# Kernel optimization log

Hardware: AMD Instinct MI355X
Metric: run time of the kernel (lower is better)

The kernel has to match this reference:

```python
import jax, jax.numpy as jnp
import numpy as np

EPS = 1e-5
C = 6          # channels (attention length)
H = 2          # heads

def _ln(x, w, b):
    mu = jnp.mean(x, axis=-1, keepdims=True)
    var = jnp.var(x, axis=-1, keepdims=True)
    return (x - mu) * jax.lax.rsqrt(var + EPS) * w + b

def setup_inputs() -> dict:
    B, N, D = 8, 4096, 768
    S = D // C           # slot_dim = 128
    key = jax.random.key(0)
    ks = jax.random.split(key, 16)
    std = 1.0 / np.sqrt(S)
    return {
        "x": jax.random.normal(ks[0], (B, N, D), jnp.float32),
        "norm1_w": jnp.ones((D,), jnp.float32),
        "norm1_b": jnp.zeros((D,), jnp.float32),
        "norm2_w": jnp.ones((S,), jnp.float32),
        "norm2_b": jnp.zeros((S,), jnp.float32),
        "qw": jax.random.normal(ks[1], (S, S), jnp.float32) * std,
        "qb": jnp.zeros((S,), jnp.float32),
        "kw": jax.random.normal(ks[2], (S, S), jnp.float32) * std,
        "kb": jnp.zeros((S,), jnp.float32),
        "vw": jax.random.normal(ks[3], (S, S), jnp.float32) * std,
        "vb": jnp.zeros((S,), jnp.float32),
        "ow": jax.random.normal(ks[4], (S, S), jnp.float32) * std,
        "ob": jnp.zeros((S,), jnp.float32),
        "ff1w": jax.random.normal(ks[5], (S, 4 * S), jnp.float32) * std,
        "ff1b": jnp.zeros((4 * S,), jnp.float32),
        "ff2w": jax.random.normal(ks[6], (4 * S, S), jnp.float32) * (std / 2),
        "ff2b": jnp.zeros((S,), jnp.float32),
    }

def reference(x, norm1_w, norm1_b, norm2_w, norm2_b,
              qw, qb, kw, kb, vw, vb, ow, ob,
              ff1w, ff1b, ff2w, ff2b):
    B, N, D = x.shape
    S = D // C
    hd = S // H
    scale = hd ** -0.5

    residual = x
    xn = _ln(x, norm1_w, norm1_b)                       # (B,N,D)
    xf = xn.reshape(B * N, C, S)                        # (M,C,S)
    xf = _ln(xf, norm2_w, norm2_b)

    # MHA over C=6 channel tokens per (B*N) slot
    M = B * N
    q = (xf @ qw + qb).reshape(M, C, H, hd)
    k = (xf @ kw + kb).reshape(M, C, H, hd)
    v = (xf @ vw + vb).reshape(M, C, H, hd)
    attn = jnp.einsum('mqhd,mkhd->mhqk', q, k) * scale  # (M,H,C,C)
    attn = jax.nn.softmax(attn, axis=-1)
    o = jnp.einsum('mhqk,mkhd->mqhd', attn, v).reshape(M, C, S)
    att_out = o @ ow + ob

    xf = xf + att_out
    ff_in = xf
    h = _ln(xf, norm2_w, norm2_b)                       # same norm2 params reused
    h = jax.nn.gelu(h @ ff1w + ff1b, approximate=False) @ ff2w + ff2b
    xf = ff_in + h

    return residual + xf.reshape(B, N, D)
```

## Files before the change

### kernel.cpp

```cpp
#include <hip/hip_runtime.h>
#include <hip/hip_bf16.h>

typedef unsigned short u16;
typedef unsigned int u32;
using bf16x8 = __attribute__((ext_vector_type(8))) short;
using f32x4  = __attribute__((ext_vector_type(4))) float;

#define LDA   136
#define SLOTS 16
#define NROWS 96

__device__ __forceinline__ u32 pk2bf(float a, float b) {
  u32 r;
  asm("v_cvt_pk_bf16_f32 %0, %1, %2" : "=v"(r) : "v"(a), "v"(b));
  return r;
}
__device__ __forceinline__ u16 f2bf(float f) { return (u16)pk2bf(f, f); }
__device__ __forceinline__ float bf2f(u16 h) {
  union { u32 u; float f; } v; v.u = ((u32)h) << 16;
  return v.f;
}
__device__ __forceinline__ float2 bf2x2(u32 u) {
  union { u32 u; float f; } a, b; a.u = u << 16; b.u = u & 0xffff0000u;
  return make_float2(a.f, b.f);
}

#if __has_builtin(__builtin_amdgcn_exp2f)
#define EXP2F(x) __builtin_amdgcn_exp2f(x)
#else
#define EXP2F(x) exp2f(x)
#endif

#define MFMA32(a, b, c) __builtin_amdgcn_mfma_f32_16x16x32_bf16(a, b, c, 0, 0, 0)

__device__ __forceinline__ float gelu_f(float x) {
  const float a = x * x;
  const float b = fmaf(-0.10294538f, a, -2.3022077f);
  const float e = EXP2F(x * b);
  return x * __builtin_amdgcn_rcpf(1.f + e);
}

__device__ __forceinline__ void handoff() {
  __builtin_amdgcn_sched_barrier(0x7F);
  asm volatile("s_waitcnt lgkmcnt(0)" ::: "memory");
  __builtin_amdgcn_sched_barrier(0x7F);
}

__global__ void convert_w(const float* __restrict__ qw, const float* __restrict__ kw,
                          const float* __restrict__ vw, const float* __restrict__ ow,
                          const float* __restrict__ f1, const float* __restrict__ f2,
                          u16* __restrict__ o) {
  int i = blockIdx.x * 256 + threadIdx.x;
  if (i < 65536) {
    int which = i >> 14;
    const float* W = which == 0 ? qw : which == 1 ? kw : which == 2 ? vw : ow;
    int t = i & 16383;
    int n = t >> 7, k = t & 127;
    o[i] = f2bf(W[k * 128 + n]);
  } else if (i < 131072) {
    int t = i - 65536;
    int n = t >> 7, k = t & 127;
    o[i] = f2bf(f1[k * 512 + n]);
  } else if (i < 196608) {
    int t = i - 131072;
    int n = t >> 9, k = t & 511;
    o[i] = f2bf(f2[k * 128 + n]);
  }
}

__device__ __forceinline__ void gemm96(const u16* __restrict__ A, const u16* __restrict__ WT,
                                       int ldw, f32x4 acc[6],
                                       int wave, int lane16, int kgrp) {
#pragma unroll
  for (int ks = 0; ks < 4; ++ks) {
    const int kk = ks * 32 + kgrp * 8;
    const bf16x8 b = *(const bf16x8*)(WT + (wave * 16 + lane16) * ldw + kk);
    __builtin_amdgcn_s_setprio(1);
#pragma unroll
    for (int xr = 0; xr < 6; ++xr) {
      const bf16x8 a = *(const bf16x8*)(A + (xr * 16 + lane16) * LDA + kk);
      acc[xr] = MFMA32(b, a, acc[xr]);
    }
    __builtin_amdgcn_s_setprio(0);
  }
}

__device__ __forceinline__ void store96(u16* __restrict__ dst, f32x4 acc[6],
                                        const float* __restrict__ bias,
                                        int wave, int lane16, int kgrp) {
  const int col0 = wave * 16 + kgrp * 4;
  const float4 bv = *(const float4*)(bias + col0);
#pragma unroll
  for (int xr = 0; xr < 6; ++xr) {
    uint2 o;
    o.x = pk2bf(acc[xr][0] + bv.x, acc[xr][1] + bv.y);
    o.y = pk2bf(acc[xr][2] + bv.z, acc[xr][3] + bv.w);
    *(uint2*)(dst + (xr * 16 + lane16) * LDA + col0) = o;
  }
}

__global__ __launch_bounds__(512) void mitra_main(
    const float* __restrict__ x,
    const float* __restrict__ nw1, const float* __restrict__ nb1,
    const float* __restrict__ nw2, const float* __restrict__ nb2,
    const float* __restrict__ qb,  const float* __restrict__ kb,
    const float* __restrict__ vb,  const float* __restrict__ ob,
    const float* __restrict__ f1b, const float* __restrict__ f2b,
    const u16* __restrict__ wt, float* __restrict__ out) {
  __shared__ u16 XF[NROWS * LDA];
  __shared__ u16 BA[NROWS * LDA];
  __shared__ u16 BB[NROWS * LDA];
  __shared__ u16 PS2[2 * NROWS * 8];

  const int tid    = threadIdx.x;
  const int wave   = tid >> 6;
  const int lane   = tid & 63;
  const int lane16 = lane & 15;
  const int kgrp   = lane >> 4;
  const long slot0 = (long)blockIdx.x * SLOTS;

#pragma unroll
  for (int si = 0; si < 2; ++si) {
    const int s = wave + si * 8;
    const float* xr = x + (size_t)(slot0 + s) * 768;
    const int l32 = lane & 31;
    float4 v[3];
    float sm = 0.f, sq = 0.f;
#pragma unroll
    for (int p = 0; p < 3; ++p) {
      v[p] = *(const float4*)(xr + (p * 64 + lane) * 4);
      sm += v[p].x + v[p].y + v[p].z + v[p].w;
      sq += v[p].x * v[p].x + v[p].y * v[p].y + v[p].z * v[p].z + v[p].w * v[p].w;
    }
#pragma unroll
    for (int m = 1; m < 64; m <<= 1) { sm += __shfl_xor(sm, m); sq += __shfl_xor(sq, m); }
    const float mu = sm * (1.f / 768.f);
    const float rs = rsqrtf(sq * (1.f / 768.f) - mu * mu + 1e-5f);
#pragma unroll
    for (int p = 0; p < 3; ++p) {
      const float4 w = *(const float4*)(nw1 + (p * 64 + lane) * 4);
      const float4 b = *(const float4*)(nb1 + (p * 64 + lane) * 4);
      v[p].x = (v[p].x - mu) * rs * w.x + b.x;
      v[p].y = (v[p].y - mu) * rs * w.y + b.y;
      v[p].z = (v[p].z - mu) * rs * w.z + b.z;
      v[p].w = (v[p].w - mu) * rs * w.w + b.w;
    }
    const float4 w2 = *(const float4*)(nw2 + l32 * 4);
    const float4 b2 = *(const float4*)(nb2 + l32 * 4);
#pragma unroll
    for (int p = 0; p < 3; ++p) {
      float s2 = v[p].x + v[p].y + v[p].z + v[p].w;
      float q2 = v[p].x * v[p].x + v[p].y * v[p].y + v[p].z * v[p].z + v[p].w * v[p].w;
#pragma unroll
      for (int m = 1; m < 32; m <<= 1) { s2 += __shfl_xor(s2, m); q2 += __shfl_xor(q2, m); }
      const float mu2 = s2 * (1.f / 128.f);
      const float rs2 = rsqrtf(q2 * (1.f / 128.f) - mu2 * mu2 + 1e-5f);
      const int row = s * 6 + 2 * p + (lane >> 5);
      uint2 o;
      o.x = pk2bf((v[p].x - mu2) * rs2 * w2.x + b2.x, (v[p].y - mu2) * rs2 * w2.y + b2.y);
      o.y = pk2bf((v[p].z - mu2) * rs2 * w2.z + b2.z, (v[p].w - mu2) * rs2 * w2.w + b2.w);
      *(uint2*)(XF + row * LDA + l32 * 4) = o;
    }
  }
  __syncthreads();

  {
    f32x4 acc[6] = {};
    gemm96(XF, wt + 0, 128, acc, wave, lane16, kgrp);
    store96(BA, acc, qb, wave, lane16, kgrp);
  }
  {
    f32x4 acc[6] = {};
    gemm96(XF, wt + 16384, 128, acc, wave, lane16, kgrp);
    store96(BB, acc, kb, wave, lane16, kgrp);
  }
  __syncthreads();

  {
#pragma unroll
    for (int jl = 0; jl < 4; ++jl) {
      const int j = wave + jl * 8;
      if (j < 28) {
        const int h  = j & 1;
        const int tt = j >> 1;
        int qt, kt;
        if (tt < 6) { qt = tt; kt = tt; }
        else {
          const int idx  = tt - 6;
          const int base = idx >> 1;
          const int lo   = base + (base >> 1);
          const int dir  = idx & 1;
          qt = lo + dir; kt = lo + 1 - dir;
        }
        f32x4 acc = {};
#pragma unroll
        for (int ks = 0; ks < 2; ++ks) {
          const int kk = h * 64 + ks * 32 + kgrp * 8;
          const bf16x8 kf = *(const bf16x8*)(BB + (kt * 16 + lane16) * LDA + kk);
          const bf16x8 qf = *(const bf16x8*)(BA + (qt * 16 + lane16) * LDA + kk);
          acc = MFMA32(kf, qf, acc);
        }
        const int q    = qt * 16 + lane16;
        const int klo  = 6 * ((unsigned)q / 6u);
        u16* pq = PS2 + (h * NROWS + q) * 8;
#pragma unroll
        for (int r = 0; r < 4; ++r) {
          const int off = kt * 16 + kgrp * 4 + r - klo;
          if ((unsigned)off < 6u) pq[off] = f2bf(acc[r] * 0.125f);
        }
      }
    }
  }
  __syncthreads();

  {
    f32x4 acc[6] = {};
    gemm96(XF, wt + 32768, 128, acc, wave, lane16, kgrp);
    store96(BA, acc, vb, wave, lane16, kgrp);
  }
  __syncthreads();

  {
    if (lane < 24) {
      const int h  = lane / 12;
      const int q  = wave * 12 + (lane % 12);
      u16* pr = PS2 + (h * NROWS + q) * 8;
      float e[6];
      float m = bf2f(pr[0]);
#pragma unroll
      for (int k = 1; k < 6; ++k) m = fmaxf(m, bf2f(pr[k]));
      float ssum = 0.f;
#pragma unroll
      for (int k = 0; k < 6; ++k) { e[k] = EXP2F((bf2f(pr[k]) - m) * 1.44269504f); ssum += e[k]; }
      const float inv = __builtin_amdgcn_rcpf(ssum);
#pragma unroll
      for (int k = 0; k < 6; ++k) pr[k] = f2bf(e[k] * inv);
    }
    handoff();

    const int dseg = lane & 15;
    const int d0   = dseg * 8;
    const int h    = dseg >> 3;
    const int rgrp = lane >> 4;
#pragma unroll
    for (int p = 0; p < 3; ++p) {
      const int rl = rgrp * 3 + p;
      const int q  = wave * 12 + rl;
      const int sl = rl / 6;
      const u16* pr = PS2 + (h * NROWS + q) * 8;
      const u16* vbase = BA + (wave * 12 + sl * 6) * LDA + d0;
      float o0 = 0, o1 = 0, o2 = 0, o3 = 0, o4 = 0, o5 = 0, o6 = 0, o7 = 0;
#pragma unroll
      for (int k = 0; k < 6; ++k) {
        const uint4 v4 = *(const uint4*)(vbase + k * LDA);
        const float pw = bf2f(pr[k]);
        const float2 a = bf2x2(v4.x), b = bf2x2(v4.y);
        const float2 c = bf2x2(v4.z), d = bf2x2(v4.w);
        o0 = fmaf(pw, a.x, o0); o1 = fmaf(pw, a.y, o1);
        o2 = fmaf(pw, b.x, o2); o3 = fmaf(pw, b.y, o3);
        o4 = fmaf(pw, c.x, o4); o5 = fmaf(pw, c.y, o5);
        o6 = fmaf(pw, d.x, o6); o7 = fmaf(pw, d.y, o7);
      }
      uint4 o;
      o.x = pk2bf(o0, o1); o.y = pk2bf(o2, o3);
      o.z = pk2bf(o4, o5); o.w = pk2bf(o6, o7);
      *(uint4*)(BB + q * LDA + d0) = o;
    }
  }
  __syncthreads();

  {
    f32x4 acc[6] = {};
    gemm96(BB, wt + 49152, 128, acc, wave, lane16, kgrp);
    const int col0 = wave * 16 + kgrp * 4;
    const float4 bv = *(const float4*)(ob + col0);
#pragma unroll
    for (int xr = 0; xr < 6; ++xr) {
      u16* px = XF + (xr * 16 + lane16) * LDA + col0;
      const uint2 cur = *(const uint2*)px;
      const float2 lo = bf2x2(cur.x), hi = bf2x2(cur.y);
      uint2 o;
      o.x = pk2bf(lo.x + acc[xr][0] + bv.x, lo.y + acc[xr][1] + bv.y);
      o.y = pk2bf(hi.x + acc[xr][2] + bv.z, hi.y + acc[xr][3] + bv.w);
      *(uint2*)px = o;
    }
  }
  __syncthreads();

  {
    const int g = tid >> 5, l32 = tid & 31;
    const float4 w2 = *(const float4*)(nw2 + l32 * 4);
    const float4 b2 = *(const float4*)(nb2 + l32 * 4);
#pragma unroll
    for (int i = 0; i < 6; ++i) {
      const int row = g * 6 + i;
      const uint2 hv = *(const uint2*)(XF + row * LDA + l32 * 4);
      const float2 lo = bf2x2(hv.x), hi = bf2x2(hv.y);
      float s2 = lo.x + lo.y + hi.x + hi.y;
      float q2 = lo.x * lo.x + lo.y * lo.y + hi.x * hi.x + hi.y * hi.y;
#pragma unroll
      for (int m = 1; m < 32; m <<= 1) { s2 += __shfl_xor(s2, m); q2 += __shfl_xor(q2, m); }
      const float mu2 = s2 * (1.f / 128.f);
      const float rs2 = rsqrtf(q2 * (1.f / 128.f) - mu2 * mu2 + 1e-5f);
      uint2 o;
      o.x = pk2bf((lo.x - mu2) * rs2 * w2.x + b2.x, (lo.y - mu2) * rs2 * w2.y + b2.y);
      o.y = pk2bf((hi.x - mu2) * rs2 * w2.z + b2.z, (hi.y - mu2) * rs2 * w2.w + b2.w);
      *(uint2*)(BA + row * LDA + l32 * 4) = o;
    }
  }

  f32x4 acc2[6];
  {
    const int col0 = wave * 16 + kgrp * 4;
#pragma unroll
    for (int xr = 0; xr < 6; ++xr) {
      const uint2 t2 = *(const uint2*)(XF + (xr * 16 + lane16) * LDA + col0);
      const float2 lo = bf2x2(t2.x), hi = bf2x2(t2.y);
      acc2[xr][0] = lo.x; acc2[xr][1] = lo.y;
      acc2[xr][2] = hi.x; acc2[xr][3] = hi.y;
    }
  }
  __syncthreads();

  {
    f32x4 g[6] = {};
    gemm96(BA, wt + 65536, 128, g, wave, lane16, kgrp);
    const int col0 = wave * 16 + kgrp * 4;
    const float4 bv = *(const float4*)(f1b + col0);
#pragma unroll
    for (int xr = 0; xr < 6; ++xr) {
      uint2 o;
      o.x = pk2bf(gelu_f(g[xr][0] + bv.x), gelu_f(g[xr][1] + bv.y));
      o.y = pk2bf(gelu_f(g[xr][2] + bv.z), gelu_f(g[xr][3] + bv.w));
      *(uint2*)(BB + (xr * 16 + lane16) * LDA + col0) = o;
    }
  }
  __syncthreads();
#pragma unroll
  for (int t = 1; t < 4; ++t) {
    u16* const Gprev = (t & 1) ? BB : XF;
    u16* const Gcur  = (t & 1) ? XF : BB;
    gemm96(Gprev, wt + 131072 + (t - 1) * 128, 512, acc2, wave, lane16, kgrp);
    f32x4 g[6] = {};
    gemm96(BA, wt + 65536 + t * 16384, 128, g, wave, lane16, kgrp);
    const int col0 = wave * 16 + kgrp * 4;
    const float4 bv = *(const float4*)(f1b + t * 128 + col0);
#pragma unroll
    for (int xr = 0; xr < 6; ++xr) {
      uint2 o;
      o.x = pk2bf(gelu_f(g[xr][0] + bv.x), gelu_f(g[xr][1] + bv.y));
      o.y = pk2bf(gelu_f(g[xr][2] + bv.z), gelu_f(g[xr][3] + bv.w));
      *(uint2*)(Gcur + (xr * 16 + lane16) * LDA + col0) = o;
    }
    __syncthreads();
  }
  gemm96(XF, wt + 131072 + 3 * 128, 512, acc2, wave, lane16, kgrp);

  {
    const int col0 = wave * 16 + kgrp * 4;
    const float4 fb = *(const float4*)(f2b + col0);
#pragma unroll
    for (int xr = 0; xr < 6; ++xr) {
      const int row  = xr * 16 + lane16;
      const int slot = row / 6, ch = row % 6;
      const size_t gi = (size_t)(slot0 + slot) * 768 + ch * 128 + col0;
      const float4 xv = *(const float4*)(x + gi);
      float4 o;
      o.x = xv.x + acc2[xr][0] + fb.x;
      o.y = xv.y + acc2[xr][1] + fb.y;
      o.z = xv.z + acc2[xr][2] + fb.z;
      o.w = xv.w + acc2[xr][3] + fb.w;
      *(float4*)(out + gi) = o;
    }
  }
}

extern "C" void kernel_launch(void* const* d_in, const int* in_sizes, int n_in,
                              void* d_out, int out_size, void* d_ws, size_t ws_size,
                              hipStream_t stream) {
  const float* x   = (const float*)d_in[0];
  const float* nw1 = (const float*)d_in[1];
  const float* nb1 = (const float*)d_in[2];
  const float* nw2 = (const float*)d_in[3];
  const float* nb2 = (const float*)d_in[4];
  const float* qw  = (const float*)d_in[5];
  const float* qb  = (const float*)d_in[6];
  const float* kw  = (const float*)d_in[7];
  const float* kb  = (const float*)d_in[8];
  const float* vw  = (const float*)d_in[9];
  const float* vb  = (const float*)d_in[10];
  const float* ow  = (const float*)d_in[11];
  const float* ob  = (const float*)d_in[12];
  const float* f1w = (const float*)d_in[13];
  const float* f1b = (const float*)d_in[14];
  const float* f2w = (const float*)d_in[15];
  const float* f2b = (const float*)d_in[16];
  u16* wt = (u16*)d_ws;

  convert_w<<<768, 256, 0, stream>>>(qw, kw, vw, ow, f1w, f2w, wt);

  const int M = in_sizes[0] / 768;
  mitra_main<<<M / SLOTS, 512, 0, stream>>>(x, nw1, nb1, nw2, nb2,
                                            qb, kb, vb, ob, f1b, f2b,
                                            wt, (float*)d_out);
}
```

Measured before the change: 180.0 us.

## Retile block GEMMs to 2 column tiles x 3 row tiles per wave

Each wave now computes a 48x32 output tile (two 16-wide column tiles and half of the 96 rows) instead of a 96x16 strip. This cuts per-wave LDS reads of the A operand in half while loading two weight fragments, which changes the LDS traffic to MFMA ratio in every GEMM stage. The softmax is also moved ahead of a barrier right after the V projection, replacing the old handoff waitcnt and removing one __syncthreads. The accumulator register count stays the same, but the access patterns change and could shift LDS bank conflicts.

```diff
diff --git a/kernel.cpp b/kernel.cpp
--- a/kernel.cpp
+++ b/kernel.cpp
@@ -38,12 +38,6 @@
   const float b = fmaf(-0.10294538f, a, -2.3022077f);
   const float e = EXP2F(x * b);
   return x * __builtin_amdgcn_rcpf(1.f + e);
-}
-
-__device__ __forceinline__ void handoff() {
-  __builtin_amdgcn_sched_barrier(0x7F);
-  asm volatile("s_waitcnt lgkmcnt(0)" ::: "memory");
-  __builtin_amdgcn_sched_barrier(0x7F);
 }
 
 __global__ void convert_w(const float* __restrict__ qw, const float* __restrict__ kw,
@@ -68,34 +62,39 @@
   }
 }
 
-__device__ __forceinline__ void gemm96(const u16* __restrict__ A, const u16* __restrict__ WT,
-                                       int ldw, f32x4 acc[6],
-                                       int wave, int lane16, int kgrp) {
+__device__ __forceinline__ void gemm96d(const u16* __restrict__ A, const u16* __restrict__ WT,
+                                        int ldw, f32x4 acc[3][2],
+                                        int cpair, int rhalf, int lane16, int kgrp) {
 #pragma unroll
   for (int ks = 0; ks < 4; ++ks) {
     const int kk = ks * 32 + kgrp * 8;
-    const bf16x8 b = *(const bf16x8*)(WT + (wave * 16 + lane16) * ldw + kk);
+    const bf16x8 b0 = *(const bf16x8*)(WT + ((cpair * 2)     * 16 + lane16) * ldw + kk);
+    const bf16x8 b1 = *(const bf16x8*)(WT + ((cpair * 2 + 1) * 16 + lane16) * ldw + kk);
     __builtin_amdgcn_s_setprio(1);
 #pragma unroll
-    for (int xr = 0; xr < 6; ++xr) {
-      const bf16x8 a = *(const bf16x8*)(A + (xr * 16 + lane16) * LDA + kk);
-      acc[xr] = MFMA32(b, a, acc[xr]);
+    for (int xr = 0; xr < 3; ++xr) {
+      const bf16x8 a = *(const bf16x8*)(A + (rhalf * 48 + xr * 16 + lane16) * LDA + kk);
+      acc[xr][0] = MFMA32(b0, a, acc[xr][0]);
+      acc[xr][1] = MFMA32(b1, a, acc[xr][1]);
     }
     __builtin_amdgcn_s_setprio(0);
   }
 }
 
-__device__ __forceinline__ void store96(u16* __restrict__ dst, f32x4 acc[6],
-                                        const float* __restrict__ bias,
-                                        int wave, int lane16, int kgrp) {
-  const int col0 = wave * 16 + kgrp * 4;
-  const float4 bv = *(const float4*)(bias + col0);
-#pragma unroll
-  for (int xr = 0; xr < 6; ++xr) {
-    uint2 o;
-    o.x = pk2bf(acc[xr][0] + bv.x, acc[xr][1] + bv.y);
-    o.y = pk2bf(acc[xr][2] + bv.z, acc[xr][3] + bv.w);
-    *(uint2*)(dst + (xr * 16 + lane16) * LDA + col0) = o;
+__device__ __forceinline__ void store96d(u16* __restrict__ dst, f32x4 acc[3][2],
+                                         const float* __restrict__ bias,
+                                         int cpair, int rhalf, int lane16, int kgrp) {
+#pragma unroll
+  for (int c = 0; c < 2; ++c) {
+    const int col0 = cpair * 32 + c * 16 + kgrp * 4;
+    const float4 bv = *(const float4*)(bias + col0);
+#pragma unroll
+    for (int xr = 0; xr < 3; ++xr) {
+      uint2 o;
+      o.x = pk2bf(acc[xr][c][0] + bv.x, acc[xr][c][1] + bv.y);
+      o.y = pk2bf(acc[xr][c][2] + bv.z, acc[xr][c][3] + bv.w);
+      *(uint2*)(dst + (rhalf * 48 + xr * 16 + lane16) * LDA + col0) = o;
+    }
   }
 }
 
@@ -117,6 +116,8 @@
   const int lane   = tid & 63;
   const int lane16 = lane & 15;
   const int kgrp   = lane >> 4;
+  const int cpair  = wave & 3;
+  const int rhalf  = wave >> 2;
   const long slot0 = (long)blockIdx.x * SLOTS;
 
 #pragma unroll
@@ -165,14 +166,14 @@
   __syncthreads();
 
   {
-    f32x4 acc[6] = {};
-    gemm96(XF, wt + 0, 128, acc, wave, lane16, kgrp);
-    store96(BA, acc, qb, wave, lane16, kgrp);
-  }
-  {
-    f32x4 acc[6] = {};
-    gemm96(XF, wt + 16384, 128, acc, wave, lane16, kgrp);
-    store96(BB, acc, kb, wave, lane16, kgrp);
+    f32x4 acc[3][2] = {};
+    gemm96d(XF, wt + 0, 128, acc, cpair, rhalf, lane16, kgrp);
+    store96d(BA, acc, qb, cpair, rhalf, lane16, kgrp);
+  }
+  {
+    f32x4 acc[3][2] = {};
+    gemm96d(XF, wt + 16384, 128, acc, cpair, rhalf, lane16, kgrp);
+    store96d(BB, acc, kb, cpair, rhalf, lane16, kgrp);
   }
   __syncthreads();
 
@@ -214,30 +215,28 @@
   __syncthreads();
 
   {
-    f32x4 acc[6] = {};
-    gemm96(XF, wt + 32768, 128, acc, wave, lane16, kgrp);
-    store96(BA, acc, vb, wave, lane16, kgrp);
-  }
-  __syncthreads();
-
-  {
-    if (lane < 24) {
-      const int h  = lane / 12;
-      const int q  = wave * 12 + (lane % 12);
-      u16* pr = PS2 + (h * NROWS + q) * 8;
-      float e[6];
-      float m = bf2f(pr[0]);
-#pragma unroll
-      for (int k = 1; k < 6; ++k) m = fmaxf(m, bf2f(pr[k]));
-      float ssum = 0.f;
-#pragma unroll
-      for (int k = 0; k < 6; ++k) { e[k] = EXP2F((bf2f(pr[k]) - m) * 1.44269504f); ssum += e[k]; }
-      const float inv = __builtin_amdgcn_rcpf(ssum);
-#pragma unroll
-      for (int k = 0; k < 6; ++k) pr[k] = f2bf(e[k] * inv);
-    }
-    handoff();
-
+    f32x4 acc[3][2] = {};
+    gemm96d(XF, wt + 32768, 128, acc, cpair, rhalf, lane16, kgrp);
+    store96d(BA, acc, vb, cpair, rhalf, lane16, kgrp);
+  }
+  if (lane < 24) {
+    const int h  = lane / 12;
+    const int q  = wave * 12 + (lane % 12);
+    u16* pr = PS2 + (h * NROWS + q) * 8;
+    float e[6];
+    float m = bf2f(pr[0]);
+#pragma unroll
+    for (int k = 1; k < 6; ++k) m = fmaxf(m, bf2f(pr[k]));
+    float ssum = 0.f;
+#pragma unroll
+    for (int k = 0; k < 6; ++k) { e[k] = EXP2F((bf2f(pr[k]) - m) * 1.44269504f); ssum += e[k]; }
+    const float inv = __builtin_amdgcn_rcpf(ssum);
+#pragma unroll
+    for (int k = 0; k < 6; ++k) pr[k] = f2bf(e[k] * inv);
+  }
+  __syncthreads();
+
+  {
     const int dseg = lane & 15;
     const int d0   = dseg * 8;
     const int h    = dseg >> 3;
@@ -270,19 +269,22 @@
   __syncthreads();
 
   {
-    f32x4 acc[6] = {};
-    gemm96(BB, wt + 49152, 128, acc, wave, lane16, kgrp);
-    const int col0 = wave * 16 + kgrp * 4;
-    const float4 bv = *(const float4*)(ob + col0);
-#pragma unroll
-    for (int xr = 0; xr < 6; ++xr) {
-      u16* px = XF + (xr * 16 + lane16) * LDA + col0;
-      const uint2 cur = *(const uint2*)px;
-      const float2 lo = bf2x2(cur.x), hi = bf2x2(cur.y);
-      uint2 o;
-      o.x = pk2bf(lo.x + acc[xr][0] + bv.x, lo.y + acc[xr][1] + bv.y);
-      o.y = pk2bf(hi.x + acc[xr][2] + bv.z, hi.y + acc[xr][3] + bv.w);
-      *(uint2*)px = o;
+    f32x4 acc[3][2] = {};
+    gemm96d(BB, wt + 49152, 128, acc, cpair, rhalf, lane16, kgrp);
+#pragma unroll
+    for (int c = 0; c < 2; ++c) {
+      const int col0 = cpair * 32 + c * 16 + kgrp * 4;
+      const float4 bv = *(const float4*)(ob + col0);
+#pragma unroll
+      for (int xr = 0; xr < 3; ++xr) {
+        u16* px = XF + (rhalf * 48 + xr * 16 + lane16) * LDA + col0;
+        const uint2 cur = *(const uint2*)px;
+        const float2 lo = bf2x2(cur.x), hi = bf2x2(cur.y);
+        uint2 o;
+        o.x = pk2bf(lo.x + acc[xr][c][0] + bv.x, lo.y + acc[xr][c][1] + bv.y);
+        o.y = pk2bf(hi.x + acc[xr][c][2] + bv.z, hi.y + acc[xr][c][3] + bv.w);
+        *(uint2*)px = o;
+      }
     }
   }
   __syncthreads();
@@ -309,30 +311,34 @@
     }
   }
 
-  f32x4 acc2[6];
-  {
-    const int col0 = wave * 16 + kgrp * 4;
-#pragma unroll
-    for (int xr = 0; xr < 6; ++xr) {
-      const uint2 t2 = *(const uint2*)(XF + (xr * 16 + lane16) * LDA + col0);
+  f32x4 acc2[3][2];
+#pragma unroll
+  for (int c = 0; c < 2; ++c) {
+    const int col0 = cpair * 32 + c * 16 + kgrp * 4;
+#pragma unroll
+    for (int xr = 0; xr < 3; ++xr) {
+      const uint2 t2 = *(const uint2*)(XF + (rhalf * 48 + xr * 16 + lane16) * LDA + col0);
       const float2 lo = bf2x2(t2.x), hi = bf2x2(t2.y);
-      acc2[xr][0] = lo.x; acc2[xr][1] = lo.y;
-      acc2[xr][2] = hi.x; acc2[xr][3] = hi.y;
-    }
-  }
-  __syncthreads();
-
-  {
-    f32x4 g[6] = {};
-    gemm96(BA, wt + 65536, 128, g, wave, lane16, kgrp);
-    const int col0 = wave * 16 + kgrp * 4;
-    const float4 bv = *(const float4*)(f1b + col0);
-#pragma unroll
-    for (int xr = 0; xr < 6; ++xr) {
-      uint2 o;
-      o.x = pk2bf(gelu_f(g[xr][0] + bv.x), gelu_f(g[xr][1] + bv.y));
-      o.y = pk2bf(gelu_f(g[xr][2] + bv.z), gelu_f(g[xr][3] + bv.w));
-      *(uint2*)(BB + (xr * 16 + lane16) * LDA + col0) = o;
+      acc2[xr][c][0] = lo.x; acc2[xr][c][1] = lo.y;
+      acc2[xr][c][2] = hi.x; acc2[xr][c][3] = hi.y;
+    }
+  }
+  __syncthreads();
+
+  {
+    f32x4 g[3][2] = {};
+    gemm96d(BA, wt + 65536, 128, g, cpair, rhalf, lane16, kgrp);
+#pragma unroll
+    for (int c = 0; c < 2; ++c) {
+      const int col0 = cpair * 32 + c * 16 + kgrp * 4;
+      const float4 bv = *(const float4*)(f1b + col0);
+#pragma unroll
+      for (int xr = 0; xr < 3; ++xr) {
+        uint2 o;
+        o.x = pk2bf(gelu_f(g[xr][c][0] + bv.x), gelu_f(g[xr][c][1] + bv.y));
+        o.y = pk2bf(gelu_f(g[xr][c][2] + bv.z), gelu_f(g[xr][c][3] + bv.w));
+        *(uint2*)(BB + (rhalf * 48 + xr * 16 + lane16) * LDA + col0) = o;
+      }
     }
   }
   __syncthreads();
@@ -340,36 +346,40 @@
   for (int t = 1; t < 4; ++t) {
     u16* const Gprev = (t & 1) ? BB : XF;
     u16* const Gcur  = (t & 1) ? XF : BB;
-    gemm96(Gprev, wt + 131072 + (t - 1) * 128, 512, acc2, wave, lane16, kgrp);
-    f32x4 g[6] = {};
-    gemm96(BA, wt + 65536 + t * 16384, 128, g, wave, lane16, kgrp);
-    const int col0 = wave * 16 + kgrp * 4;
-    const float4 bv = *(const float4*)(f1b + t * 128 + col0);
-#pragma unroll
-    for (int xr = 0; xr < 6; ++xr) {
-      uint2 o;
-      o.x = pk2bf(gelu_f(g[xr][0] + bv.x), gelu_f(g[xr][1] + bv.y));
-      o.y = pk2bf(gelu_f(g[xr][2] + bv.z), gelu_f(g[xr][3] + bv.w));
-      *(uint2*)(Gcur + (xr * 16 + lane16) * LDA + col0) = o;
+    gemm96d(Gprev, wt + 131072 + (t - 1) * 128, 512, acc2, cpair, rhalf, lane16, kgrp);
+    f32x4 g[3][2] = {};
+    gemm96d(BA, wt + 65536 + t * 16384, 128, g, cpair, rhalf, lane16, kgrp);
+#pragma unroll
+    for (int c = 0; c < 2; ++c) {
+      const int col0 = cpair * 32 + c * 16 + kgrp * 4;
+      const float4 bv = *(const float4*)(f1b + t * 128 + col0);
+#pragma unroll
+      for (int xr = 0; xr < 3; ++xr) {
+        uint2 o;
+        o.x = pk2bf(gelu_f(g[xr][c][0] + bv.x), gelu_f(g[xr][c][1] + bv.y));
+        o.y = pk2bf(gelu_f(g[xr][c][2] + bv.z), gelu_f(g[xr][c][3] + bv.w));
+        *(uint2*)(Gcur + (rhalf * 48 + xr * 16 + lane16) * LDA + col0) = o;
+      }
     }
     __syncthreads();
   }
-  gemm96(XF, wt + 131072 + 3 * 128, 512, acc2, wave, lane16, kgrp);
-
-  {
-    const int col0 = wave * 16 + kgrp * 4;
+  gemm96d(XF, wt + 131072 + 3 * 128, 512, acc2, cpair, rhalf, lane16, kgrp);
+
+#pragma unroll
+  for (int c = 0; c < 2; ++c) {
+    const int col0 = cpair * 32 + c * 16 + kgrp * 4;
     const float4 fb = *(const float4*)(f2b + col0);
 #pragma unroll
-    for (int xr = 0; xr < 6; ++xr) {
-      const int row  = xr * 16 + lane16;
+    for (int xr = 0; xr < 3; ++xr) {
+      const int row  = rhalf * 48 + xr * 16 + lane16;
       const int slot = row / 6, ch = row % 6;
       const size_t gi = (size_t)(slot0 + slot) * 768 + ch * 128 + col0;
       const float4 xv = *(const float4*)(x + gi);
       float4 o;
-      o.x = xv.x + acc2[xr][0] + fb.x;
-      o.y = xv.y + acc2[xr][1] + fb.y;
-      o.z = xv.z + acc2[xr][2] + fb.z;
-      o.w = xv.w + acc2[xr][3] + fb.w;
+      o.x = xv.x + acc2[xr][c][0] + fb.x;
+      o.y = xv.y + acc2[xr][c][1] + fb.y;
+      o.z = xv.z + acc2[xr][c][2] + fb.z;
+      o.w = xv.w + acc2[xr][c][3] + fb.w;
       *(float4*)(out + gi) = o;
     }
   }
```

Result: slower. 239.1 us (+32.8%).
